# Kernel optimization log

Hardware: AMD Instinct MI355X
Metric: run time of the kernel (lower is better)

The kernel has to match this reference:

```python
import jax, jax.numpy as jnp
import numpy as np

H = 12      # num_heads
EPS = 1e-5  # LayerNorm eps (torch default)


def _ln(x, g, b):
    m = x.mean(-1, keepdims=True)
    v = x.var(-1, keepdims=True)
    return (x - m) * jax.lax.rsqrt(v + EPS) * g + b


def _rot_half(x):
    x1, x2 = x[..., 0::2], x[..., 1::2]
    return jnp.stack((-x2, x1), axis=-1).reshape(x.shape)


def _rope_tables(n, head_dim):
    # rotary-embedding-torch: RotaryEmbedding(dim=head_dim//2, use_xpos=True),
    # theta=10000, scale_base=512. Only first rot=head_dim//2 dims are rotated.
    rot = head_dim // 2
    inv = 1.0 / (10000.0 ** (jnp.arange(0, rot, 2, dtype=jnp.float32) / rot))
    t = jnp.arange(n, dtype=jnp.float32)
    freqs = jnp.repeat(t[:, None] * inv[None, :], 2, axis=-1)  # (n, rot), interleaved
    base = (jnp.arange(0, rot, 2, dtype=jnp.float32) + 0.4 * rot) / (1.4 * rot)
    power = (t - n // 2) / 512.0
    sc = base[None, :] ** power[:, None]
    sc = jnp.concatenate([sc, sc], axis=-1)  # (n, rot), concatenated (library behavior)
    return jnp.cos(freqs), jnp.sin(freqs), sc


def _attn_path(xn, Wqkv, bqkv, Wproj, bproj, qg, qb, kg, kb, R, rg, rb):
    B, N, D = xn.shape
    d = D // H
    qkv = xn @ Wqkv + bqkv
    q, k, v = jnp.split(qkv, 3, axis=-1)
    hd = lambda t: t.reshape(B, N, H, d).transpose(0, 2, 1, 3)  # (B,H,N,d)
    q, k, v = hd(q), hd(k), hd(v)
    q = _ln(q, qg, qb)  # per-head QK LayerNorm
    k = _ln(k, kg, kb)
    cos, sin, sc = _rope_tables(N, d)
    rot = d // 2

    def rope(t, s):  # rotate only first rot dims
        tl, tr = t[..., :rot], t[..., rot:]
        tl = tl * cos * s + _rot_half(tl) * sin * s
        return jnp.concatenate([tl, tr], axis=-1)

    q = rope(q, sc)
    v = rope(v, 1.0 / sc)  # source applies rope to (q, v), not k

    scores = jnp.einsum('bhid,bhjd->bhij', q, k) / jnp.sqrt(jnp.asarray(d, xn.dtype))
    p = jax.nn.softmax(scores, axis=-1)
    # SDPA(q,k,ones_NN)[...,i,j] == sum_k p[...,i,k] for every j (constant over j).
    # All downstream ops (head-mix einsum, LayerNorm over heads, @ v) therefore
    # reduce exactly to the per-(b,i) computation below, avoiding an N^3 matmul.
    s = p.sum(-1)                              # (B,H,N)
    mix = jnp.einsum('bhi,hg->big', s, R)      # (B,N,H)
    w = _ln(mix, rg, rb)                       # reattn LayerNorm over head axis
    vsum = v.sum(axis=2)                       # (B,H,d); (w @ v) with w const over j
    y = jnp.einsum('big,bgd->bigd', w, vsum).reshape(B, N, D)
    return y @ Wproj + bproj


def _cgmlp(xn, W1, b1, gg, gb, cw, cb, W2, b2):
    h = jax.nn.gelu(xn @ W1 + b1, approximate=False)
    c2 = h.shape[-1] // 2
    xr, xg = h[..., :c2], h[..., c2:]
    xg = _ln(xg, gg, gb).transpose(0, 2, 1)  # (B,C,T)
    K = cw.shape[-1]
    xg = jax.lax.conv_general_dilated(xg, cw, (1,), [((K - 1) // 2, (K - 1) // 2)],
                                      dimension_numbers=('NCH', 'OIH', 'NCH'),
                                      feature_group_count=c2)  # depthwise conv1d
    xg = (xg + cb[None, :, None]).transpose(0, 2, 1)
    return (xr * xg) @ W2 + b2


def reference(x, Wqkv, bqkv, Wproj, bproj, qn_g, qn_b, kn_g, kn_b, reattn_w, rn_g, rn_b,
              ln1_g, ln1_b, ln2_g, ln2_b, ls1, ls2, W1, b1, gn_g, gn_b, conv_w, conv_b,
              W2, b2, Wout, bout):
    # eval mode: dropout / drop_path are identity
    xa = _ln(x, ln1_g, ln1_b)
    attn = sum(_attn_path(xa, Wqkv[p], bqkv[p], Wproj[p], bproj[p], qn_g[p], qn_b[p],
                          kn_g[p], kn_b[p], reattn_w[p], rn_g[p], rn_b[p])
               for p in range(2))
    x_attn = x + ls1 * attn
    xm = _ln(x, ln2_g, ln2_b)
    x_mlp = x + ls2 * _cgmlp(xm, W1, b1, gn_g, gn_b, conv_w, conv_b, W2, b2)
    xf = jnp.concatenate([x_attn, x_mlp], axis=-1)
    return xf @ Wout + bout + x


def setup_inputs():
    B, N, D, P = 4, 1024, 768, 2
    d = D // H
    C = 4 * D
    c2 = C // 2
    K = 21
    ks = iter(jax.random.split(jax.random.key(0), 16))
    nrm = lambda s, sd=0.02: jax.random.normal(next(ks), s, jnp.float32) * sd
    return {
        'x': jax.random.normal(next(ks), (B, N, D), jnp.float32),
        'Wqkv': nrm((P, D, 3 * D)), 'bqkv': jnp.zeros((P, 3 * D)),
        'Wproj': nrm((P, D, D)), 'bproj': jnp.zeros((P, D)),
        'qn_g': jnp.ones((P, d)), 'qn_b': jnp.zeros((P, d)),
        'kn_g': jnp.ones((P, d)), 'kn_b': jnp.zeros((P, d)),
        'reattn_w': jax.random.normal(next(ks), (P, H, H), jnp.float32),
        'rn_g': jnp.ones((P, H)), 'rn_b': jnp.zeros((P, H)),
        'ln1_g': jnp.ones((D,)), 'ln1_b': jnp.zeros((D,)),
        'ln2_g': jnp.ones((D,)), 'ln2_b': jnp.zeros((D,)),
        'ls1': jnp.full((D,), 0.01, jnp.float32), 'ls2': jnp.full((D,), 0.01, jnp.float32),
        'W1': nrm((D, C)), 'b1': jnp.zeros((C,)),
        'gn_g': jnp.ones((c2,)), 'gn_b': jnp.zeros((c2,)),
        'conv_w': nrm((c2, 1, K), 0.1), 'conv_b': jnp.zeros((c2,)),
        'W2': nrm((c2, D)), 'b2': jnp.zeros((D,)),
        'Wout': nrm((2 * D, D)), 'bout': jnp.zeros((D,)),
    }
```

## Files before the change

kernel.cpp:

```cpp
#include <hip/hip_runtime.h>
#include <hip/hip_bf16.h>

typedef short s16x8 __attribute__((ext_vector_type(8)));
typedef float f32x4 __attribute__((ext_vector_type(4)));

#define C2 1536

__device__ __forceinline__ float b2f(ushort u){ return __uint_as_float(((unsigned)u)<<16); }
__device__ __forceinline__ ushort f2b(float f){ unsigned u = __float_as_uint(f); return (ushort)((u + 0x7fffu + ((u>>16)&1u)) >> 16); }

#define GL16(g, l) __builtin_amdgcn_global_load_lds( \
    (const __attribute__((address_space(1))) void*)(g), \
    (__attribute__((address_space(3))) void*)(l), 16, 0, 0)

#define VMW(n) asm volatile("s_waitcnt vmcnt(" #n ")" ::: "memory")
#define LGW()  asm volatile("s_waitcnt lgkmcnt(0)" ::: "memory")
#define SB()   __builtin_amdgcn_sched_barrier(0)
#define BAR()  __builtin_amdgcn_s_barrier()
#define SP1    __builtin_amdgcn_s_setprio(1)
#define SP0    __builtin_amdgcn_s_setprio(0)
#define MF(va, vb, c) __builtin_amdgcn_mfma_f32_16x16x32_bf16(va, vb, c, 0,0,0)

#define RDA(P, mh) { const int ab = (P) + aro + (mh)*4096; \
    a0=L8(ab+sx0);      a1=L8(ab+sx1); \
    a2=L8(ab+1024+sx0); a3=L8(ab+1024+sx1); \
    a4=L8(ab+2048+sx0); a5=L8(ab+2048+sx1); \
    a6=L8(ab+3072+sx0); a7=L8(ab+3072+sx1); }
#define RDB0(P, nh) { const int bb = (P) + bro + (nh)*2048; \
    b00=L8(bb+sx0); b01=L8(bb+sx1); b02=L8(bb+1024+sx0); b03=L8(bb+1024+sx1); }
#define RDB1(P, nh) { const int bb = (P) + bro + (nh)*2048; \
    b10=L8(bb+sx0); b11=L8(bb+sx1); b12=L8(bb+1024+sx0); b13=L8(bb+1024+sx1); }
#define L8(off) (*(const s16x8*)&lds[off])
#define STG(p0, p1, T, dstb) { \
    GL16((p0) + (size_t)(T)*64, &lds[(dstb) + ldsw]); \
    GL16((p1) + (size_t)(T)*64, &lds[(dstb) + 4096 + ldsw]); }
#define QD(mh, nh, B0,B1,B2,B3) { \
  acc[(mh)*4+0][(nh)*2+0]=MF(a0,B0,acc[(mh)*4+0][(nh)*2+0]); \
  acc[(mh)*4+0][(nh)*2+0]=MF(a1,B1,acc[(mh)*4+0][(nh)*2+0]); \
  acc[(mh)*4+0][(nh)*2+1]=MF(a0,B2,acc[(mh)*4+0][(nh)*2+1]); \
  acc[(mh)*4+0][(nh)*2+1]=MF(a1,B3,acc[(mh)*4+0][(nh)*2+1]); \
  acc[(mh)*4+1][(nh)*2+0]=MF(a2,B0,acc[(mh)*4+1][(nh)*2+0]); \
  acc[(mh)*4+1][(nh)*2+0]=MF(a3,B1,acc[(mh)*4+1][(nh)*2+0]); \
  acc[(mh)*4+1][(nh)*2+1]=MF(a2,B2,acc[(mh)*4+1][(nh)*2+1]); \
  acc[(mh)*4+1][(nh)*2+1]=MF(a3,B3,acc[(mh)*4+1][(nh)*2+1]); \
  acc[(mh)*4+2][(nh)*2+0]=MF(a4,B0,acc[(mh)*4+2][(nh)*2+0]); \
  acc[(mh)*4+2][(nh)*2+0]=MF(a5,B1,acc[(mh)*4+2][(nh)*2+0]); \
  acc[(mh)*4+2][(nh)*2+1]=MF(a4,B2,acc[(mh)*4+2][(nh)*2+1]); \
  acc[(mh)*4+2][(nh)*2+1]=MF(a5,B3,acc[(mh)*4+2][(nh)*2+1]); \
  acc[(mh)*4+3][(nh)*2+0]=MF(a6,B0,acc[(mh)*4+3][(nh)*2+0]); \
  acc[(mh)*4+3][(nh)*2+0]=MF(a7,B1,acc[(mh)*4+3][(nh)*2+0]); \
  acc[(mh)*4+3][(nh)*2+1]=MF(a6,B2,acc[(mh)*4+3][(nh)*2+1]); \
  acc[(mh)*4+3][(nh)*2+1]=MF(a7,B3,acc[(mh)*4+3][(nh)*2+1]); }

#define EIGHT(t0, t1, DS, VM4) \
   VMW(4); BAR(); \
  RDA(0,0); RDB0(0,0); \
  STG(pA00,pA01,(t1), 16384); \
  LGW(); SB(); SP1; QD(0,0,b00,b01,b02,b03); SP0; BAR(); \
   RDB1(0,1); \
  STG(pA10,pA11,(t1), 24576); \
  BAR(); LGW(); SB(); SP1; QD(0,1,b10,b11,b12,b13); SP0; BAR(); \
   RDA(0,1); \
  if (DS) { STG(pB00,pB01,(t0)+2, 32768); } \
  BAR(); LGW(); SB(); SP1; QD(1,0,b00,b01,b02,b03); SP0; BAR(); \
   if (DS) { STG(pB10,pB11,(t0)+2, 40960); } \
  BAR(); SP1; QD(1,1,b10,b11,b12,b13); SP0; BAR(); \
   VM4; BAR(); \
  RDA(16384,0); RDB0(16384,0); \
  if (DS) { STG(pA00,pA01,(t0)+2, 0); } \
  LGW(); SB(); SP1; QD(0,0,b00,b01,b02,b03); SP0; BAR(); \
   RDB1(16384,1); \
  if (DS) { STG(pA10,pA11,(t0)+2, 8192); } \
  BAR(); LGW(); SB(); SP1; QD(0,1,b10,b11,b12,b13); SP0; BAR(); \
   RDA(16384,1); \
  if (DS) { STG(pB00,pB01,(t1)+2, 49152); } \
  BAR(); LGW(); SB(); SP1; QD(1,0,b00,b01,b02,b03); SP0; BAR(); \
   if (DS) { STG(pB10,pB11,(t1)+2, 57344); } \
  BAR(); SP1; QD(1,1,b10,b11,b12,b13); SP0; BAR();

template<int EPI>
__global__ __launch_bounds__(512, 1) void gemm256(
    const ushort* __restrict__ A, const ushort* __restrict__ BT,
    int M, int N, int K,
    const float* __restrict__ bias,
    ushort* __restrict__ o16, ushort* __restrict__ o16b)
{
    extern __shared__ ushort lds[];
    const int t = threadIdx.x;
    const int lane = t & 63, wv = t >> 6;
    const int wr = wv >> 2, wc = wv & 3;
    const int r0 = lane & 15, q = lane >> 4, e7 = lane & 7;
    const int m0 = blockIdx.y*256, n0 = blockIdx.x*256;

    const int idx = wv*64 + lane;
    const int lr8 = idx >> 3;
    const int ksrc = (idx & 7) ^ (lr8 & 7);
    const ushort* pA00 = A  + (size_t)(m0 +   0 +  0 + lr8)*K + ksrc*8;
    const ushort* pA01 = A  + (size_t)(m0 +   0 + 64 + lr8)*K + ksrc*8;
    const ushort* pA10 = A  + (size_t)(m0 + 128 +  0 + lr8)*K + ksrc*8;
    const ushort* pA11 = A  + (size_t)(m0 + 128 + 64 + lr8)*K + ksrc*8;
    const ushort* pB00 = BT + (size_t)(n0 +   0 +  0 + lr8)*K + ksrc*8;
    const ushort* pB01 = BT + (size_t)(n0 +   0 + 64 + lr8)*K + ksrc*8;
    const ushort* pB10 = BT + (size_t)(n0 + 128 +  0 + lr8)*K + ksrc*8;
    const ushort* pB11 = BT + (size_t)(n0 + 128 + 64 + lr8)*K + ksrc*8;
    const int ldsw = wv*512;

    const int aro = (wr*128 + r0)*64;
    const int bro = 32768 + (wc*64 + r0)*64;
    const int sx0 = (q ^ e7)*8, sx1 = ((q ^ e7)*8) ^ 32;

    f32x4 acc[8][4];
    #pragma unroll
    for (int i=0;i<8;++i)
        #pragma unroll
        for (int j=0;j<4;++j) acc[i][j] = (f32x4){0.f,0.f,0.f,0.f};
    s16x8 a0,a1,a2,a3,a4,a5,a6,a7;
    s16x8 b00,b01,b02,b03, b10,b11,b12,b13;

    const int nkt = K >> 6;
    const int niter = nkt >> 1;

    STG(pB00,pB01, 0, 32768);
    STG(pB10,pB11, 0, 40960);
    STG(pA00,pA01, 0, 0);
    STG(pA10,pA11, 0, 8192);
    STG(pB00,pB01, 1, 49152);
    STG(pB10,pB11, 1, 57344);

    for (int i = 0; i < niter-1; ++i) {
        const int t0 = 2*i, t1 = 2*i+1;
        EIGHT(t0, t1, 1, VMW(4));
    }
    {
        const int t0 = nkt-2, t1 = nkt-1;
        EIGHT(t0, t1, 0, VMW(0));
    }

    #pragma unroll
    for (int gm=0; gm<8; ++gm) {
        #pragma unroll
        for (int gn=0; gn<4; ++gn) {
            int col = n0 + wc*64 + gn*16 + r0;
            #pragma unroll
            for (int r=0; r<4; ++r) {
                int row = m0 + wr*128 + gm*16 + q*4 + r;
                float v = acc[gm][gn][r];
                if (EPI == 0) {
                    o16[(size_t)row*N + col] = f2b(v + bias[col]);
                } else {
                    v += bias[col];
                    float g = 0.5f*v*(1.0f + erff(v*0.70710678118f));
                    if (col < C2) o16 [(size_t)row*C2 + col]        = f2b(g);
                    else          o16b[(size_t)row*C2 + (col - C2)] = f2b(g);
                }
            }
        }
    }
}

template<int EPI>
__global__ __launch_bounds__(256) void gemm_bf16(
    const ushort* __restrict__ A, const ushort* __restrict__ BT,
    int M, int N, int K, int lda, int ldbt,
    const float* __restrict__ bias, const float* __restrict__ xres,
    const float* __restrict__ w1tp, const float* __restrict__ w2tp, float* __restrict__ vsump,
    ushort* __restrict__ o16, float* __restrict__ o32)
{
    __shared__ ushort Al[2][128*32];
    __shared__ ushort Bl[2][128*32];
    const int t = threadIdx.x;
    const int m0 = blockIdx.y*128, n0 = blockIdx.x*128;
    const int lane = t & 63, wv = t >> 6;
    const int wm = (wv>>1)*64, wn = (wv&1)*64;
    const int r0 = lane & 15, q = lane >> 4;

    const int c0i = t, c1i = t + 256;
    const int lrow0 = ((c0i>>6)<<4) | (c0i&15), lkc0 = ((c0i>>4)&3) << 3;
    const int lrow1 = ((c1i>>6)<<4) | (c1i&15), lkc1 = ((c1i>>4)&3) << 3;
    const ushort* gA0 = A  + (size_t)(m0+lrow0)*lda + lkc0;
    const ushort* gB0 = BT + (size_t)(n0+lrow0)*ldbt + lkc0;
    const ushort* gA1 = A  + (size_t)(m0+lrow1)*lda + lkc1;
    const ushort* gB1 = BT + (size_t)(n0+lrow1)*ldbt + lkc1;

    f32x4 acc[4][4];
    #pragma unroll
    for (int i=0;i<4;++i)
        #pragma unroll
        for (int j=0;j<4;++j) acc[i][j] = (f32x4){0.f,0.f,0.f,0.f};

    const int nkt = K >> 5;
    uint4 pa0_0, pb0_0, pa1_0, pb1_0;
    uint4 pa0_1, pb0_1, pa1_1, pb1_1;
    pa0_0 = *(const uint4*)gA0;        pb0_0 = *(const uint4*)gB0;
    pa1_0 = *(const uint4*)gA1;        pb1_0 = *(const uint4*)gB1;
    pa0_1 = *(const uint4*)(gA0 + 32); pb0_1 = *(const uint4*)(gB0 + 32);
    pa1_1 = *(const uint4*)(gA1 + 32); pb1_1 = *(const uint4*)(gB1 + 32);
    *(uint4*)&Al[0][c0i*8] = pa0_0;
    *(uint4*)&Bl[0][c0i*8] = pb0_0;
    *(uint4*)&Al[0][c1i*8] = pa1_0;
    *(uint4*)&Bl[0][c1i*8] = pb1_0;

    for (int kt = 0; kt < nkt; kt += 2) {
        __syncthreads();
        {
            s16x8 af[4], bfr[4];
            #pragma unroll
            for (int mt=0; mt<4; ++mt) af[mt]  = *(const s16x8*)&Al[0][(((wm>>4)+mt)*64 + lane)*8];
            #pragma unroll
            for (int nt=0; nt<4; ++nt) bfr[nt] = *(const s16x8*)&Bl[0][(((wn>>4)+nt)*64 + lane)*8];
            *(uint4*)&Al[1][c0i*8] = pa0_1;
            *(uint4*)&Bl[1][c0i*8] = pb0_1;
            *(uint4*)&Al[1][c1i*8] = pa1_1;
            *(uint4*)&Bl[1][c1i*8] = pb1_1;
            if (kt+2 < nkt) {
                pa0_0 = *(const uint4*)(gA0 + (kt+2)*32);
                pb0_0 = *(const uint4*)(gB0 + (kt+2)*32);
                pa1_0 = *(const uint4*)(gA1 + (kt+2)*32);
                pb1_0 = *(const uint4*)(gB1 + (kt+2)*32);
            }
            #pragma unroll
            for (int mt=0; mt<4; ++mt)
                #pragma unroll
                for (int nt=0; nt<4; ++nt)
                    acc[mt][nt] = __builtin_amdgcn_mfma_f32_16x16x32_bf16(af[mt], bfr[nt], acc[mt][nt], 0,0,0);
        }
        __syncthreads();
        {
            s16x8 af[4], bfr[4];
            #pragma unroll
            for (int mt=0; mt<4; ++mt) af[mt]  = *(const s16x8*)&Al[1][(((wm>>4)+mt)*64 + lane)*8];
            #pragma unroll
            for (int nt=0; nt<4; ++nt) bfr[nt] = *(const s16x8*)&Bl[1][(((wn>>4)+nt)*64 + lane)*8];
            if (kt+2 < nkt) {
                *(uint4*)&Al[0][c0i*8] = pa0_0;
                *(uint4*)&Bl[0][c0i*8] = pb0_0;
                *(uint4*)&Al[0][c1i*8] = pa1_0;
                *(uint4*)&Bl[0][c1i*8] = pb1_0;
            }
            if (kt+3 < nkt) {
                pa0_1 = *(const uint4*)(gA0 + (kt+3)*32);
                pb0_1 = *(const uint4*)(gB0 + (kt+3)*32);
                pa1_1 = *(const uint4*)(gA1 + (kt+3)*32);
                pb1_1 = *(const uint4*)(gB1 + (kt+3)*32);
            }
            #pragma unroll
            for (int mt=0; mt<4; ++mt)
                #pragma unroll
                for (int nt=0; nt<4; ++nt)
                    acc[mt][nt] = __builtin_amdgcn_mfma_f32_16x16x32_bf16(af[mt], bfr[nt], acc[mt][nt], 0,0,0);
        }
    }

    if (EPI == 0) {
        float cs0=0.f, cs1=0.f, cs2=0.f, cs3=0.f;
        #pragma unroll
        for (int mt=0; mt<4; ++mt) {
            #pragma unroll
            for (int r=0; r<4; ++r) {
                int row = m0 + wm + mt*16 + q*4 + r;
                int ii = (row & 1023) << 6;
                #pragma unroll
                for (int nt=0; nt<4; ++nt) {
                    int col = n0 + wn + nt*16 + r0;
                    float vb = acc[mt][nt][r] + bias[col];
                    float vn = __shfl_xor(vb, 1, 64);
                    float c = w1tp[ii + (col & 63)]*vb + w2tp[ii + (col & 63)]*vn;
                    if (nt == 0) cs0 += c; else if (nt == 1) cs1 += c;
                    else if (nt == 2) cs2 += c; else cs3 += c;
                }
            }
        }
        cs0 += __shfl_xor(cs0, 16, 64); cs0 += __shfl_xor(cs0, 32, 64);
        cs1 += __shfl_xor(cs1, 16, 64); cs1 += __shfl_xor(cs1, 32, 64);
        cs2 += __shfl_xor(cs2, 16, 64); cs2 += __shfl_xor(cs2, 32, 64);
        cs3 += __shfl_xor(cs3, 16, 64); cs3 += __shfl_xor(cs3, 32, 64);
        if (lane < 16) {
            int b = m0 >> 10;
            atomicAdd(&vsump[b*1536 + n0 + wn +  0 + lane], cs0);
            atomicAdd(&vsump[b*1536 + n0 + wn + 16 + lane], cs1);
            atomicAdd(&vsump[b*1536 + n0 + wn + 32 + lane], cs2);
            atomicAdd(&vsump[b*1536 + n0 + wn + 48 + lane], cs3);
        }
    } else {
        #pragma unroll
        for (int mt=0; mt<4; ++mt) {
            #pragma unroll
            for (int nt=0; nt<4; ++nt) {
                int col = n0 + wn + nt*16 + r0;
                #pragma unroll
                for (int r=0; r<4; ++r) {
                    int row = m0 + wm + mt*16 + q*4 + r;
                    float v = acc[mt][nt][r];
                    if (EPI == 3) {
                        o32[(size_t)row*768 + col] = v + bias[(row>>10)*768 + col] + xres[(size_t)row*768 + col];
                    } else {
                        o16[(size_t)row*2304 + 768 + col] = f2b(v);
                    }
                }
            }
        }
    }
}

__global__ __launch_bounds__(256) void mega_prep(
    const float* __restrict__ Wqkv, const float* __restrict__ W1,
    const float* __restrict__ Wout, const float* __restrict__ W2,
    const float* __restrict__ ls2,  const float* __restrict__ bqkv,
    const float* __restrict__ x,
    const float* __restrict__ g1, const float* __restrict__ b1v,
    const float* __restrict__ g2, const float* __restrict__ b2v,
    const float* __restrict__ R,  const float* __restrict__ rng,
    const float* __restrict__ rnb, const float* __restrict__ bproj,
    const float* __restrict__ bout,
    ushort* __restrict__ WvT, ushort* __restrict__ W1T, ushort* __restrict__ BTf,
    ushort* __restrict__ Afold, ushort* __restrict__ BT2, float* __restrict__ bvp,
    float* __restrict__ w1t, float* __restrict__ w2t, float* __restrict__ wvec,
    float* __restrict__ attn_c, float* __restrict__ vsum, float* __restrict__ cvecb,
    ushort* __restrict__ xa, ushort* __restrict__ xm, ushort* __restrict__ xc)
{
    __shared__ float tl[32*33];
    const int blk = blockIdx.x;
    const int t = threadIdx.x;

    if (blk < 1152) {
        int p = blk / 576, l = blk % 576;
        int kt = (l % 24)*32, nt = (l / 24)*32;
        const float* src = Wqkv + (size_t)p*768*2304;
        ushort* dst = WvT + (size_t)p*768*768;
        int nl = t & 31, kg = t >> 5;
        #pragma unroll
        for (int kk=0; kk<4; ++kk) {
            int k = kg*4 + kk;
            tl[k*33 + nl] = src[(size_t)(kt + k)*2304 + 1536 + nt + nl];
        }
        __syncthreads();
        int kcol = t & 31, ng = t >> 5;
        #pragma unroll
        for (int nn=0; nn<4; ++nn) {
            int nrow = ng*4 + nn;
            dst[(size_t)(nt + nrow)*768 + kt + kcol] = f2b(tl[kcol*33 + nrow]);
        }
    } else if (blk < 3456) {
        int l = blk - 1152;
        int kt = (l % 24)*32, nt = (l / 24)*32;
        int nl = t & 31, kg = t >> 5;
        #pragma unroll
        for (int kk=0; kk<4; ++kk) {
            int k = kg*4 + kk;
            tl[k*33 + nl] = W1[(size_t)(kt + k)*3072 + nt + nl];
        }
        __syncthreads();
        int kcol = t & 31, ng = t >> 5;
        #pragma unroll
        for (int nn=0; nn<4; ++nn) {
            int nrow = ng*4 + nn;
            W1T[(size_t)(nt + nrow)*768 + kt + kcol] = f2b(tl[kcol*33 + nrow]);
        }
    } else if (blk < 4032) {
        int l = blk - 3456;
        int kt = (l % 24)*32, nt = (l / 24)*32;
        int nl = t & 31, kg = t >> 5;
        #pragma unroll
        for (int kk=0; kk<4; ++kk) {
            int k = kg*4 + kk;
            tl[k*33 + nl] = Wout[(size_t)(kt + k)*768 + nt + nl]
                          + Wout[(size_t)(768 + kt + k)*768 + nt + nl];
        }
        __syncthreads();
        int kcol = t & 31, ng = t >> 5;
        #pragma unroll
        for (int nn=0; nn<4; ++nn) {
            int nrow = ng*4 + nn;
            BTf[(size_t)(nt + nrow)*2304 + kt + kcol] = f2b(tl[kcol*33 + nrow]);
        }
    } else if (blk < 4608) {
        int l = blk - 4032;
        int kt = (l % 24)*32, nt = (l / 24)*32;
        const float* src = Wout + (size_t)768*768;
        int nl = t & 31, kg = t >> 5;
        #pragma unroll
        for (int kk=0; kk<4; ++kk) {
            int k = kg*4 + kk;
            tl[k*33 + nl] = src[(size_t)(kt + k)*768 + nt + nl];
        }
        __syncthreads();
        int kcol = t & 31, ng = t >> 5;
        #pragma unroll
        for (int nn=0; nn<4; ++nn) {
            int nrow = ng*4 + nn;
            Afold[(size_t)(nt + nrow)*768 + kt + kcol] = f2b(tl[kcol*33 + nrow] * ls2[kt + kcol]);
        }
    } else if (blk < 9216) {
        int i = (blk - 4608)*256 + t;
        BT2[i] = f2b(W2[i]);
    } else if (blk < 9222) {
        int i = (blk - 9216)*256 + t;
        if (i < 1536) bvp[i] = bqkv[(i/768)*2304 + 1536 + (i%768)];
    } else if (blk < 9478) {
        int pb = blk - 9222;
        int idx = pb*256 + t;
        {
            int i = idx >> 6, j = idx & 63;
            float w1, w2;
            if (j < 32) {
                int m = j >> 1;
                float inv = powf(10000.f, -(float)m*(1.f/16.f));
                float fr = (float)i * inv;
                float c = cosf(fr), sn = sinf(fr);
                float power = ((float)i - 512.f) * (1.f/512.f);
                float basev = (2.f*(float)(j & 15) + 12.8f) * (1.f/44.8f);
                float sfac = powf(basev, -power);
                w1 = c * sfac;
                w2 = ((j & 1) ? sn : -sn) * sfac;
            } else { w1 = 1.f; w2 = 0.f; }
            w1t[idx] = w1; w2t[idx] = w2;
        }
        if (pb >= 1 && pb <= 12) {
            int k = (pb-1)*256 + t;
            int o = k % 768;
            attn_c[k] = bproj[o] + bproj[768 + o];
        }
        if (pb >= 13 && pb <= 36) {
            int k = (pb-13)*256 + t;
            vsum[k] = 0.f;
        }
        if (pb >= 37 && pb <= 48) {
            int k = (pb-37)*256 + t;
            cvecb[k] = bout[k % 768];
        }
        if (pb == 0) {
            float* mixs = tl;
            float* wsb  = tl + 32;
            if (t < 24) {
                int p = t / 12, g = t % 12;
                float m = 0.f;
                for (int h=0; h<12; ++h) m += R[p*144 + h*12 + g];
                mixs[t] = m;
            }
            __syncthreads();
            if (t < 2) {
                float mean=0.f, var=0.f;
                for (int g=0; g<12; ++g) mean += mixs[t*12+g];
                mean *= (1.f/12.f);
                for (int g=0; g<12; ++g){ float d = mixs[t*12+g]-mean; var += d*d; }
                var *= (1.f/12.f);
                float rstd = rsqrtf(var + 1e-5f);
                for (int g=0; g<12; ++g)
                    wsb[t*12+g] = (mixs[t*12+g]-mean)*rstd*rng[t*12+g] + rnb[t*12+g];
            }
            __syncthreads();
            if (t < 24) wvec[t] = wsb[t];
        }
    } else {
        int row = blk - 9478;
        float* sb = tl;
        float v[3]; float s = 0.f, ss = 0.f;
        #pragma unroll
        for (int e=0; e<3; ++e) { v[e] = x[(size_t)row*768 + t + e*256]; s += v[e]; ss += v[e]*v[e]; }
        for (int o=32; o>0; o>>=1){ s += __shfl_down(s,o,64); ss += __shfl_down(ss,o,64); }
        int lane = t&63, w = t>>6;
        if (lane==0){ sb[w]=s; sb[4+w]=ss; }
        __syncthreads();
        s = sb[0]+sb[1]+sb[2]+sb[3]; ss = sb[4]+sb[5]+sb[6]+sb[7];
        float mean = s*(1.f/768.f);
        float var  = ss*(1.f/768.f) - mean*mean;
        float rstd = rsqrtf(var + 1e-5f);
        #pragma unroll
        for (int e=0; e<3; ++e){
            int c = t + e*256;
            float n = (v[e]-mean)*rstd;
            xa[(size_t)row*768 + c] = f2b(n*g1[c] + b1v[c]);
            xm[(size_t)row*768 + c] = f2b(n*g2[c] + b2v[c]);
            xc[(size_t)row*2304 + c] = f2b(v[e]);
        }
    }
}

__global__ __launch_bounds__(256) void attn_gemm(const float* __restrict__ vsum,
    const float* __restrict__ wvec, const float* __restrict__ Wproj, float* __restrict__ attn_c)
{
    int o  = blockIdx.x*256 + threadIdx.x;
    int c0 = blockIdx.y * 96;
    int b  = blockIdx.z;
    int p  = c0 / 768;
    float acc = 0.f;
    #pragma unroll 4
    for (int cc=0; cc<96; ++cc) {
        int c = c0 + cc;
        int cl = c - p*768;
        float y = wvec[p*12 + (cl>>6)] * vsum[b*1536 + c];
        acc += y * Wproj[(size_t)p*589824 + (size_t)cl*768 + o];
    }
    atomicAdd(&attn_c[b*768 + o], acc);
}

__global__ __launch_bounds__(256) void cvec_kernel(const float* __restrict__ attn_c,
    const float* __restrict__ ls1, const float* __restrict__ ls2, const float* __restrict__ b2,
    const float* __restrict__ Wout, float* __restrict__ cvecb)
{
    int o  = blockIdx.x*256 + threadIdx.x;
    int r0 = blockIdx.y * 96;
    int b  = blockIdx.z;
    float acc = 0.f;
    #pragma unroll 4
    for (int rr = 0; rr < 96; ++rr) {
        int r = r0 + rr;
        float coef = (r < 768) ? ls1[r]*attn_c[b*768 + r]
                               : ls2[r-768]*b2[r-768];
        acc += coef * Wout[(size_t)r*768 + o];
    }
    atomicAdd(&cvecb[b*768 + o], acc);
}

__global__ __launch_bounds__(256) void ln_stats(const ushort* __restrict__ xg,
    float2* __restrict__ stats)
{
    __shared__ float sb[8];
    int row = blockIdx.x, t = threadIdx.x;
    float s=0.f, ss=0.f;
    #pragma unroll
    for (int e=0;e<6;++e){ float v = b2f(xg[(size_t)row*1536 + t + e*256]); s+=v; ss+=v*v; }
    for (int o=32; o>0; o>>=1){ s += __shfl_down(s,o,64); ss += __shfl_down(ss,o,64); }
    int lane = t&63, w = t>>6;
    if (lane==0){ sb[w]=s; sb[4+w]=ss; }
    __syncthreads();
    s = sb[0]+sb[1]+sb[2]+sb[3]; ss = sb[4]+sb[5]+sb[6]+sb[7];
    float mean = s*(1.f/1536.f);
    float var  = ss*(1.f/1536.f) - mean*mean;
    if (t == 0) stats[row] = make_float2(mean, rsqrtf(var + 1e-5f));
}

#define CROWS 128
#define CIN   (CROWS + 20)
#define CSTR  72
__global__ __launch_bounds__(256) void conv_mul(const ushort* __restrict__ xg,
    const float2* __restrict__ stats,
    const float* __restrict__ gg, const float* __restrict__ gb,
    const float* __restrict__ cw, const float* __restrict__ cb,
    const ushort* __restrict__ xr, ushort* __restrict__ u)
{
    __shared__ ushort tile[CIN * CSTR];
    const int c0 = blockIdx.x * 64;
    const int i0 = blockIdx.y * CROWS;
    const int b  = blockIdx.z;
    const int t  = threadIdx.x;
    const size_t base = (size_t)b*1024*1536;

    #pragma unroll
    for (int it = 0; it < 5; ++it) {
        int idx = it*256 + t;
        if (idx < CIN*8) {
            int r  = idx >> 3;
            int cq = (idx & 7) * 8;
            int si = i0 + r - 10;
            uint4 val = make_uint4(0u,0u,0u,0u);
            if (si >= 0 && si < 1024) {
                uint4 raw = *(const uint4*)(xg + base + (size_t)si*1536 + c0 + cq);
                float2 st = stats[b*1024 + si];
                const ushort* rp = (const ushort*)&raw;
                ushort* vp = (ushort*)&val;
                #pragma unroll
                for (int e=0; e<8; ++e) {
                    int c = c0 + cq + e;
                    vp[e] = f2b((b2f(rp[e]) - st.x)*st.y*gg[c] + gb[c]);
                }
            }
            *(uint4*)&tile[r*CSTR + cq] = val;
        }
    }
    __syncthreads();

    const int ch = t & 63;
    const int o0 = (t >> 6) * 32;
    const int c  = c0 + ch;

    float w[21];
    #pragma unroll
    for (int k=0; k<21; ++k) w[k] = cw[c*21 + k];
    const float bias = cb[c];

    float win[21];
    #pragma unroll
    for (int j=0; j<20; ++j) win[j] = b2f(tile[(o0+j)*CSTR + ch]);

    #pragma unroll
    for (int j=0; j<32; ++j) {
        win[(j+20)%21] = b2f(tile[(o0+j+20)*CSTR + ch]);
        float acc = bias;
        #pragma unroll
        for (int k=0; k<21; ++k) acc += win[(j+k)%21] * w[k];
        size_t offr = base + (size_t)(i0+o0+j)*1536 + c;
        u[(size_t)(b*1024 + i0+o0+j)*2304 + 768 + c] = f2b(b2f(xr[offr]) * acc);
    }
}

extern "C" void kernel_launch(void* const* d_in, const int* in_sizes, int n_in,
                              void* d_out, int out_size, void* d_ws, size_t ws_size,
                              hipStream_t stream)
{
    const float* x     = (const float*)d_in[0];
    const float* Wqkv  = (const float*)d_in[1];
    const float* bqkv  = (const float*)d_in[2];
    const float* Wproj = (const float*)d_in[3];
    const float* bproj = (const float*)d_in[4];
    const float* Rw    = (const float*)d_in[9];
    const float* rng   = (const float*)d_in[10];
    const float* rnb   = (const float*)d_in[11];
    const float* ln1g  = (const float*)d_in[12];
    const float* ln1b  = (const float*)d_in[13];
    const float* ln2g  = (const float*)d_in[14];
    const float* ln2b  = (const float*)d_in[15];
    const float* ls1   = (const float*)d_in[16];
    const float* ls2   = (const float*)d_in[17];
    const float* W1    = (const float*)d_in[18];
    const float* b1    = (const float*)d_in[19];
    const float* gng   = (const float*)d_in[20];
    const float* gnb   = (const float*)d_in[21];
    const float* cw    = (const float*)d_in[22];
    const float* cb    = (const float*)d_in[23];
    const float* W2    = (const float*)d_in[24];
    const float* b2    = (const float*)d_in[25];
    const float* Wout  = (const float*)d_in[26];
    const float* bout  = (const float*)d_in[27];
    float* out = (float*)d_out;

    char* ws = (char*)d_ws;
    size_t off = 0;
    auto alloc = [&](size_t bytes)->char* {
        char* p = ws + off;
        off += (bytes + 255) & ~(size_t)255;
        return p;
    };
    ushort* WvT   = (ushort*)alloc(1536*768*2);
    ushort* W1T   = (ushort*)alloc(3072*768*2);
    ushort* BT2   = (ushort*)alloc(1536*768*2);
    ushort* Afold = (ushort*)alloc(768*768*2);
    ushort* BTf   = (ushort*)alloc(768*2304*2);
    float*  bvp   = (float*)alloc(1536*4);
    float*  w1t   = (float*)alloc(65536*4);
    float*  w2t   = (float*)alloc(65536*4);
    float*  wvec  = (float*)alloc(24*4);
    float*  attnc = (float*)alloc(3072*4);
    float*  vsum  = (float*)alloc(6144*4);
    float*  cvecb = (float*)alloc(3072*4);
    float2* stats = (float2*)alloc(4096*8);
    ushort* xa16  = (ushort*)alloc(4096*768*2);
    ushort* xm16  = (ushort*)alloc(4096*768*2);
    ushort* xr16  = (ushort*)alloc(4096*1536*2);
    ushort* xg16  = (ushort*)alloc(4096*1536*2);
    ushort* xcat  = (ushort*)alloc((size_t)4096*2304*2);
    (void)ws_size; (void)n_in; (void)in_sizes; (void)out_size;

    (void)hipFuncSetAttribute((const void*)gemm256<1>, hipFuncAttributeMaxDynamicSharedMemorySize, 131072);

    mega_prep<<<dim3(13574), 256, 0, stream>>>(
        Wqkv, W1, Wout, W2, ls2, bqkv, x,
        ln1g, ln1b, ln2g, ln2b, Rw, rng, rnb, bproj, bout,
        WvT, W1T, BTf, Afold, BT2, bvp,
        w1t, w2t, wvec, attnc, vsum, cvecb,
        xa16, xm16, xcat);

    gemm_bf16<4><<<dim3(12, 6), 256, 0, stream>>>(Afold, BT2, 768, 1536, 768, 768, 768,
                                                  nullptr, nullptr, nullptr, nullptr, nullptr,
                                                  BTf, nullptr);

    gemm_bf16<0><<<dim3(12, 32), 256, 0, stream>>>(xa16, WvT, 4096, 1536, 768, 768, 768,
                                                   bvp, nullptr, w1t, w2t, vsum,
                                                   nullptr, nullptr);
    attn_gemm<<<dim3(3, 16, 4), 256, 0, stream>>>(vsum, wvec, Wproj, attnc);
    cvec_kernel<<<dim3(3, 16, 4), 256, 0, stream>>>(attnc, ls1, ls2, b2, Wout, cvecb);

    gemm256<1><<<dim3(12, 16), 512, 131072, stream>>>(xm16, W1T, 4096, 3072, 768,
                                                      b1, xr16, xg16);
    ln_stats<<<dim3(4096), 256, 0, stream>>>(xg16, stats);
    conv_mul<<<dim3(24, 8, 4), 256, 0, stream>>>(xg16, stats, gng, gnb, cw, cb, xr16, xcat);

    gemm_bf16<3><<<dim3(6, 32), 256, 0, stream>>>(xcat, BTf, 4096, 768, 2304, 2304, 2304,
                                                  cvecb, x, nullptr, nullptr, nullptr,
                                                  nullptr, out);
}
```

Baseline: 325.3 us.

## Split-K the value and output GEMMs and add a separate combine kernel

```diff
diff --git a/kernel.cpp b/kernel.cpp
--- a/kernel.cpp
+++ b/kernel.cpp
@@ -162,14 +162,15 @@
 __global__ __launch_bounds__(256) void gemm_bf16(
     const ushort* __restrict__ A, const ushort* __restrict__ BT,
     int M, int N, int K, int lda, int ldbt,
-    const float* __restrict__ bias, const float* __restrict__ xres,
+    const float* __restrict__ bias,
     const float* __restrict__ w1tp, const float* __restrict__ w2tp, float* __restrict__ vsump,
-    ushort* __restrict__ o16, float* __restrict__ o32)
+    ushort* __restrict__ o16, float* __restrict__ o32, float* __restrict__ o32b)
 {
     __shared__ ushort Al[2][128*32];
     __shared__ ushort Bl[2][128*32];
     const int t = threadIdx.x;
     const int m0 = blockIdx.y*128, n0 = blockIdx.x*128;
+    const int koff = blockIdx.z * K;
     const int lane = t & 63, wv = t >> 6;
     const int wm = (wv>>1)*64, wn = (wv&1)*64;
     const int r0 = lane & 15, q = lane >> 4;
@@ -177,10 +178,10 @@
     const int c0i = t, c1i = t + 256;
     const int lrow0 = ((c0i>>6)<<4) | (c0i&15), lkc0 = ((c0i>>4)&3) << 3;
     const int lrow1 = ((c1i>>6)<<4) | (c1i&15), lkc1 = ((c1i>>4)&3) << 3;
-    const ushort* gA0 = A  + (size_t)(m0+lrow0)*lda + lkc0;
-    const ushort* gB0 = BT + (size_t)(n0+lrow0)*ldbt + lkc0;
-    const ushort* gA1 = A  + (size_t)(m0+lrow1)*lda + lkc1;
-    const ushort* gB1 = BT + (size_t)(n0+lrow1)*ldbt + lkc1;
+    const ushort* gA0 = A  + (size_t)(m0+lrow0)*lda + koff + lkc0;
+    const ushort* gB0 = BT + (size_t)(n0+lrow0)*ldbt + koff + lkc0;
+    const ushort* gA1 = A  + (size_t)(m0+lrow1)*lda + koff + lkc1;
+    const ushort* gB1 = BT + (size_t)(n0+lrow1)*ldbt + koff + lkc1;
 
     f32x4 acc[4][4];
     #pragma unroll
@@ -252,6 +253,7 @@
     }
 
     if (EPI == 0) {
+        const bool kz0 = (blockIdx.z == 0);
         float cs0=0.f, cs1=0.f, cs2=0.f, cs3=0.f;
         #pragma unroll
         for (int mt=0; mt<4; ++mt) {
@@ -262,7 +264,7 @@
                 #pragma unroll
                 for (int nt=0; nt<4; ++nt) {
                     int col = n0 + wn + nt*16 + r0;
-                    float vb = acc[mt][nt][r] + bias[col];
+                    float vb = acc[mt][nt][r] + (kz0 ? bias[col] : 0.f);
                     float vn = __shfl_xor(vb, 1, 64);
                     float c = w1tp[ii + (col & 63)]*vb + w2tp[ii + (col & 63)]*vn;
                     if (nt == 0) cs0 += c; else if (nt == 1) cs1 += c;
@@ -282,6 +284,7 @@
             atomicAdd(&vsump[b*1536 + n0 + wn + 48 + lane], cs3);
         }
     } else {
+        float* pd = (EPI == 6) ? (blockIdx.z ? o32b : o32) : nullptr;
         #pragma unroll
         for (int mt=0; mt<4; ++mt) {
             #pragma unroll
@@ -291,8 +294,8 @@
                 for (int r=0; r<4; ++r) {
                     int row = m0 + wm + mt*16 + q*4 + r;
                     float v = acc[mt][nt][r];
-                    if (EPI == 3) {
-                        o32[(size_t)row*768 + col] = v + bias[(row>>10)*768 + col] + xres[(size_t)row*768 + col];
+                    if (EPI == 6) {
+                        pd[(size_t)row*768 + col] = v;
                     } else {
                         o16[(size_t)row*2304 + 768 + col] = f2b(v);
                     }
@@ -300,6 +303,25 @@
             }
         }
     }
+}
+
+__global__ __launch_bounds__(256) void combine_out(const float* __restrict__ p0,
+    const float* __restrict__ p1, const float* __restrict__ cvecb,
+    const float* __restrict__ x, float* __restrict__ out)
+{
+    size_t i = ((size_t)blockIdx.x*256 + threadIdx.x)*4;
+    int col = (int)(i % 768);
+    int b   = (int)((i / 768) >> 10);
+    float4 a  = *(const float4*)(p0 + i);
+    float4 bq = *(const float4*)(p1 + i);
+    float4 xx = *(const float4*)(x + i);
+    const float* cv = cvecb + b*768 + col;
+    float4 r;
+    r.x = a.x + bq.x + xx.x + cv[0];
+    r.y = a.y + bq.y + xx.y + cv[1];
+    r.z = a.z + bq.z + xx.z + cv[2];
+    r.w = a.w + bq.w + xx.w + cv[3];
+    *(float4*)(out + i) = r;
 }
 
 __global__ __launch_bounds__(256) void mega_prep(
@@ -480,12 +502,12 @@
     const float* __restrict__ wvec, const float* __restrict__ Wproj, float* __restrict__ attn_c)
 {
     int o  = blockIdx.x*256 + threadIdx.x;
-    int c0 = blockIdx.y * 96;
+    int c0 = blockIdx.y * 48;
     int b  = blockIdx.z;
     int p  = c0 / 768;
     float acc = 0.f;
     #pragma unroll 4
-    for (int cc=0; cc<96; ++cc) {
+    for (int cc=0; cc<48; ++cc) {
         int c = c0 + cc;
         int cl = c - p*768;
         float y = wvec[p*12 + (cl>>6)] * vsum[b*1536 + c];
@@ -499,11 +521,11 @@
     const float* __restrict__ Wout, float* __restrict__ cvecb)
 {
     int o  = blockIdx.x*256 + threadIdx.x;
-    int r0 = blockIdx.y * 96;
+    int r0 = blockIdx.y * 48;
     int b  = blockIdx.z;
     float acc = 0.f;
     #pragma unroll 4
-    for (int rr = 0; rr < 96; ++rr) {
+    for (int rr = 0; rr < 48; ++rr) {
         int r = r0 + rr;
         float coef = (r < 768) ? ls1[r]*attn_c[b*768 + r]
                                : ls2[r-768]*b2[r-768];
@@ -649,6 +671,8 @@
     ushort* xr16  = (ushort*)alloc(4096*1536*2);
     ushort* xg16  = (ushort*)alloc(4096*1536*2);
     ushort* xcat  = (ushort*)alloc((size_t)4096*2304*2);
+    float* p0 = (float*)xa16;
+    float* p1 = (float*)xg16;
     (void)ws_size; (void)n_in; (void)in_sizes; (void)out_size;
 
     (void)hipFuncSetAttribute((const void*)gemm256<1>, hipFuncAttributeMaxDynamicSharedMemorySize, 131072);
@@ -661,21 +685,22 @@
         xa16, xm16, xcat);
 
     gemm_bf16<4><<<dim3(12, 6), 256, 0, stream>>>(Afold, BT2, 768, 1536, 768, 768, 768,
-                                                  nullptr, nullptr, nullptr, nullptr, nullptr,
-                                                  BTf, nullptr);
-
-    gemm_bf16<0><<<dim3(12, 32), 256, 0, stream>>>(xa16, WvT, 4096, 1536, 768, 768, 768,
-                                                   bvp, nullptr, w1t, w2t, vsum,
-                                                   nullptr, nullptr);
-    attn_gemm<<<dim3(3, 16, 4), 256, 0, stream>>>(vsum, wvec, Wproj, attnc);
-    cvec_kernel<<<dim3(3, 16, 4), 256, 0, stream>>>(attnc, ls1, ls2, b2, Wout, cvecb);
+                                                  nullptr, nullptr, nullptr, nullptr,
+                                                  BTf, nullptr, nullptr);
+
+    gemm_bf16<0><<<dim3(12, 32, 2), 256, 0, stream>>>(xa16, WvT, 4096, 1536, 384, 768, 768,
+                                                      bvp, w1t, w2t, vsum,
+                                                      nullptr, nullptr, nullptr);
+    attn_gemm<<<dim3(3, 32, 4), 256, 0, stream>>>(vsum, wvec, Wproj, attnc);
+    cvec_kernel<<<dim3(3, 32, 4), 256, 0, stream>>>(attnc, ls1, ls2, b2, Wout, cvecb);
 
     gemm256<1><<<dim3(12, 16), 512, 131072, stream>>>(xm16, W1T, 4096, 3072, 768,
                                                       b1, xr16, xg16);
     ln_stats<<<dim3(4096), 256, 0, stream>>>(xg16, stats);
     conv_mul<<<dim3(24, 8, 4), 256, 0, stream>>>(xg16, stats, gng, gnb, cw, cb, xr16, xcat);
 
-    gemm_bf16<3><<<dim3(6, 32), 256, 0, stream>>>(xcat, BTf, 4096, 768, 2304, 2304, 2304,
-                                                  cvecb, x, nullptr, nullptr, nullptr,
-                                                  nullptr, out);
-}
+    gemm_bf16<6><<<dim3(6, 32, 2), 256, 0, stream>>>(xcat, BTf, 4096, 768, 1152, 2304, 2304,
+                                                     nullptr, nullptr, nullptr, nullptr,
+                                                     nullptr, p0, p1);
+    combine_out<<<dim3(3072), 256, 0, stream>>>(p0, p1, cvecb, x, out);
+}
```

After: 435.8 us. 1.34x slower.
